# Performance work log

Hardware: AMD Instinct MI355X
Metric: run time of the kernel (lower is better)

Reference implementation:

```python
import jax, jax.numpy as jnp
import numpy as np


def lstm_cell(x, h, c, Wih, Whh, bih, bhh):
    # PyTorch LSTM gate order: i, f, g, o
    gates = x @ Wih.T + h @ Whh.T + bih + bhh
    i, f, g, o = jnp.split(gates, 4, axis=-1)
    c_new = jax.nn.sigmoid(f) * c + jax.nn.sigmoid(i) * jnp.tanh(g)
    h_new = jax.nn.sigmoid(o) * jnp.tanh(c_new)
    return h_new, c_new


def setup_inputs() -> dict:
    V, E, H, L, S, B, T = 100000, 256, 256, 2, 256, 16, 128
    G = 4 * H
    s = 0.1  # weight scale to keep activations/gradients well-conditioned
    key = jax.random.key(0)
    ks = jax.random.split(key, 16)
    return {
        'source': jax.random.randint(ks[0], (S, B), 0, V),
        'target_size': T,
        'target_embeddings': jax.random.normal(ks[1], (T, 1, E), dtype=jnp.float32),
        'h0': jax.random.normal(ks[2], (L, B, H), dtype=jnp.float32) * s,
        'c0': jax.random.normal(ks[3], (L, B, H), dtype=jnp.float32) * s,
        'embed_table': jax.random.normal(ks[4], (V, E), dtype=jnp.float32) * s,
        'enc_Wih': jax.random.normal(ks[5], (L, G, E), dtype=jnp.float32) * s,
        'enc_Whh': jax.random.normal(ks[6], (L, G, H), dtype=jnp.float32) * s,
        'enc_bih': jax.random.normal(ks[7], (L, G), dtype=jnp.float32) * s,
        'enc_bhh': jax.random.normal(ks[8], (L, G), dtype=jnp.float32) * s,
        'dec_Wih': jax.random.normal(ks[9], (L, G, E), dtype=jnp.float32) * s,
        'dec_Whh': jax.random.normal(ks[10], (L, G, H), dtype=jnp.float32) * s,
        'dec_bih': jax.random.normal(ks[11], (L, G), dtype=jnp.float32) * s,
        'dec_bhh': jax.random.normal(ks[12], (L, G), dtype=jnp.float32) * s,
        'attn_W': jax.random.normal(ks[13], (1, 2 * H), dtype=jnp.float32) * s,
        'attn_b': jnp.zeros((1,), dtype=jnp.float32),
        'comb_W': jax.random.normal(ks[14], (H, 2 * H), dtype=jnp.float32) * s,
        'comb_b': jnp.zeros((H,), dtype=jnp.float32),
    }


def reference(source, target_size, target_embeddings, h0, c0, embed_table,
              enc_Wih, enc_Whh, enc_bih, enc_bhh,
              dec_Wih, dec_Whh, dec_bih, dec_bhh,
              attn_W, attn_b, comb_W, comb_b):
    L = h0.shape[0]
    B = source.shape[1]

    # ---------------- encoder (per-step LSTM loop -> layer-wise scans) ----
    x = embed_table[source]  # [S, B, E]  (dropout is identity at eval)
    h_fin = []
    for l in range(L):
        def step(carry, xt, l=l):
            h, c = carry
            h, c = lstm_cell(xt, h, c, enc_Wih[l], enc_Whh[l], enc_bih[l], enc_bhh[l])
            return (h, c), h
        (hL, cL), x = jax.lax.scan(step, (h0[l], c0[l]), x)
        h_fin.append(hL)
    hidden_final = jnp.stack(h_fin)   # [L, B, H] == hiddens[-1] in the source
    enc_outputs = x                   # [S, B, H] last-layer hidden per step
    S = enc_outputs.shape[0]

    # NOTE (faithful to source bugs): seq2seq sets both decoder hidden AND
    # cell from encoder_hidden[-1], and the decoder runs its LSTM on the raw
    # input `embedding`, discarding the attention-combined output.
    x0 = jnp.tile(target_embeddings[0, 0], (B, 1))  # [B, E]

    def dec_step(carry, _):
        x, h, c = carry
        # per-step Bahdanau-style attention: computed but UNUSED, as in source
        cat = jnp.concatenate([jnp.broadcast_to(x, (S,) + x.shape), enc_outputs], axis=-1)
        w = jax.nn.softmax(cat @ attn_W.T + attn_b, axis=0)       # [S, B, 1]
        applied = (w * enc_outputs).sum(0)                         # [B, H]
        _combined = jax.nn.relu(jnp.concatenate([x, applied], axis=-1) @ comb_W.T + comb_b)
        # actual recurrence: multi-layer LSTM on the raw input x
        inp = x
        hs, cs = [], []
        for l in range(h.shape[0]):
            hl, cl = lstm_cell(inp, h[l], c[l], dec_Wih[l], dec_Whh[l], dec_bih[l], dec_bhh[l])
            hs.append(hl)
            cs.append(cl)
            inp = hl
        return (inp, jnp.stack(hs), jnp.stack(cs)), inp

    _, ys = jax.lax.scan(dec_step, (x0, hidden_final, hidden_final), None,
                         length=target_size - 1)  # ys: [T-1, B, H]
    H = ys.shape[-1]
    preds = jnp.zeros((target_size, 1, B, H), ys.dtype)
    preds = preds.at[1:].set(ys[:, None])  # predictions[0] stays zero
    return preds
```

## Files before the change

kernel.cpp:

```cpp
#include <hip/hip_runtime.h>
#include <hip/hip_bf16.h>

typedef __attribute__((ext_vector_type(8))) short short8;
typedef __attribute__((ext_vector_type(4))) float f32x4;

#define SEQ   256
#define BB    16
#define EE    256
#define HH    256
#define GG    1024
#define TT    128
#define NWG   32
#define KP    264
#define SLOT_S 8192
#define SENT  0xFF80FF80u
#define MAXTRY (1 << 20)

__device__ __forceinline__ float sigm(float x) { return 1.0f / (1.0f + __expf(-x)); }
__device__ __forceinline__ float tanh_f(float x) {
    float e = __expf(2.0f * x);
    return 1.0f - 2.0f / (e + 1.0f);
}
__device__ __forceinline__ void split2s(float v, short* hi, short* lo) {
    __hip_bfloat16 h = __float2bfloat16(v);
    __hip_bfloat16 l = __float2bfloat16(v - __bfloat162float(h));
    *hi = *(short*)&h; *lo = *(short*)&l;
}
__device__ __forceinline__ f32x4 MFMA(short8 a, short8 b, f32x4 c) {
    return __builtin_amdgcn_mfma_f32_16x16x32_bf16(a, b, c, 0, 0, 0);
}

__device__ __forceinline__ short8 ld16s(const short* p) {
    short8 r;
    asm volatile("global_load_dwordx4 %0, %1, off sc0 sc1" : "=v"(r) : "v"(p));
    return r;
}
__device__ __forceinline__ int ld4f(const int* p) {
    int r;
    asm volatile("global_load_dword %0, %1, off sc0 sc1\n\ts_waitcnt vmcnt(0)"
                 : "=v"(r) : "v"(p) : "memory");
    return r;
}
__device__ __forceinline__ void st4s(int* p, int v) {
    asm volatile("global_store_dword %0, %1, off sc0 sc1" :: "v"(p), "v"(v) : "memory");
}
__device__ __forceinline__ void vmwait() {
    asm volatile("s_waitcnt vmcnt(0)" ::: "memory");
    __builtin_amdgcn_sched_barrier(0);
}
__device__ __forceinline__ void sync_lds() {
    __builtin_amdgcn_sched_barrier(0);
    asm volatile("s_waitcnt lgkmcnt(0)" ::: "memory");
    __builtin_amdgcn_s_barrier();
    __builtin_amdgcn_sched_barrier(0);
}
union U8 { short8 s; unsigned u[4]; };
__device__ __forceinline__ unsigned chk(short8 f) {
    U8 x; x.s = f;
    return (unsigned)((x.u[0] == SENT) | (x.u[1] == SENT) | (x.u[2] == SENT) | (x.u[3] == SENT));
}

__global__ void k_sent(unsigned* p) {
    long i = ((long)blockIdx.x * 256 + threadIdx.x) * 4;
    p[i] = SENT; p[i + 1] = SENT; p[i + 2] = SENT; p[i + 3] = SENT;
}

__global__ void k_cvt4(const float* __restrict__ s0, const float* __restrict__ s1,
                       const float* __restrict__ s2, const float* __restrict__ s3,
                       char* __restrict__ ws) {
    int g = blockIdx.x >> 11;
    int i = (blockIdx.x & 2047) * 256 + threadIdx.x;
    const float* s = (g == 0) ? s0 : (g == 1) ? s1 : (g == 2) ? s2 : s3;
    __hip_bfloat16* hi = (__hip_bfloat16*)(ws + ((size_t)2 * g) * (1u << 20));
    __hip_bfloat16* lo = (__hip_bfloat16*)(ws + ((size_t)2 * g + 1) * (1u << 20));
    short a, b; split2s(s[i], &a, &b);
    hi[i] = *(__hip_bfloat16*)&a; lo[i] = *(__hip_bfloat16*)&b;
}

__global__ void k_embed(const int* __restrict__ src, const float* __restrict__ tab,
                        __hip_bfloat16* __restrict__ xhi, __hip_bfloat16* __restrict__ xlo) {
    int r = blockIdx.x;
    int j = threadIdx.x;
    long idx = src[r];
    short a, b; split2s(tab[idx * EE + j], &a, &b);
    xhi[(long)r * EE + j] = *(__hip_bfloat16*)&a;
    xlo[(long)r * EE + j] = *(__hip_bfloat16*)&b;
}

__global__ void __launch_bounds__(256) k_gemm_in(
        const __hip_bfloat16* __restrict__ Xhi, const __hip_bfloat16* __restrict__ Xlo,
        const __hip_bfloat16* __restrict__ Whi, const __hip_bfloat16* __restrict__ Wlo,
        const float* __restrict__ bih, const float* __restrict__ bhh,
        float* __restrict__ gates) {
    int lane = threadIdx.x & 63, w = threadIdx.x >> 6;
    int m0 = (blockIdx.x >> 4) * 16;
    int n0 = ((blockIdx.x & 15) * 4 + w) * 16;
    int cc = lane & 15, g = lane >> 4;
    int koff = g * 8;
    const short* xh = (const short*)Xhi + (long)(m0 + cc) * EE + koff;
    const short* xl = (const short*)Xlo + (long)(m0 + cc) * EE + koff;
    const short* wh = (const short*)Whi + (long)(n0 + cc) * EE + koff;
    const short* wl = (const short*)Wlo + (long)(n0 + cc) * EE + koff;
    f32x4 acc1 = {0.f, 0.f, 0.f, 0.f}, acc2 = {0.f, 0.f, 0.f, 0.f};
#pragma unroll
    for (int k = 0; k < EE; k += 32) {
        short8 ah = *(const short8*)(xh + k), al = *(const short8*)(xl + k);
        short8 bh = *(const short8*)(wh + k), bl = *(const short8*)(wl + k);
        acc1 = MFMA(ah, bh, acc1);
        acc2 = MFMA(ah, bl, acc2);
        acc2 = MFMA(al, bh, acc2);
    }
    f32x4 acc = acc1 + acc2;
    int ncol = n0 + cc;
    float bias = bih[ncol] + bhh[ncol];
    int jj = ncol & 255, qq = ncol >> 8;
    int mrow = m0 + g * 4;
#pragma unroll
    for (int r = 0; r < 4; ++r)
        gates[(long)(mrow + r) * GG + jj * 4 + qq] = acc[r] + bias;
}

__device__ __forceinline__ void load_wslice(const short* __restrict__ Wg, int j0,
                                            short* __restrict__ Wl) {
    int tid = threadIdx.x;
    int lr = tid >> 3;
    int q = lr >> 3, jl = lr & 7;
    const short* src = Wg + (long)(q * 256 + j0 + jl) * 256;
    short* dst = Wl + lr * KP;
#pragma unroll
    for (int s = 0; s < 4; ++s) {
        int c = (tid & 7) * 8 + s * 64;
        *(short8*)(dst + c) = *(const short8*)(src + c);
    }
}


__global__ void __launch_bounds__(256, 1) k_enc_coop(
        const float* __restrict__ gates0,
        const short* __restrict__ Whh0h, const short* __restrict__ Whh0l,
        const short* __restrict__ Wih1h, const short* __restrict__ Wih1l,
        const short* __restrict__ Whh1h, const short* __restrict__ Whh1l,
        const float* __restrict__ bih1, const float* __restrict__ bhh1,
        const float* __restrict__ h0p, const float* __restrict__ c0p,
        short* __restrict__ H0, short* __restrict__ H1,
        float* __restrict__ hfin,
        int* __restrict__ FE0, int* __restrict__ FE1) {
    __shared__ short Wl[6][32 * KP];
    __shared__ float gacc[2][8][16][17];

    int tid = threadIdx.x, bid = blockIdx.x;
    int j0 = bid * 8;
    load_wslice(Whh0h, j0, Wl[0]); load_wslice(Whh0l, j0, Wl[1]);
    load_wslice(Wih1h, j0, Wl[2]); load_wslice(Wih1l, j0, Wl[3]);
    load_wslice(Whh1h, j0, Wl[4]); load_wslice(Whh1l, j0, Wl[5]);

    int bb = (tid & 127) >> 3, jl = tid & 7, j = j0 + jl, lay = tid >> 7;
    float creg = c0p[lay * 4096 + bb * 256 + j];
    float bs[4] = {0.f, 0.f, 0.f, 0.f};
    if (lay) {
#pragma unroll
        for (int q = 0; q < 4; ++q) bs[q] = bih1[q * 256 + j] + bhh1[q * 256 + j];
    }
    f32x4 gnew = {0.f, 0.f, 0.f, 0.f};
    if (!lay) {
        gnew = *(const f32x4*)(gates0 + ((long)bb * 256 + j) * 4);
    }
    {
        float hv = h0p[lay * 4096 + bb * 256 + j];
        short sh, sl; split2s(hv, &sh, &sl);
        int mh = (unsigned short)sh, ml = (unsigned short)sl;
        int nh = __shfl_down(mh, 1), nl = __shfl_down(ml, 1);
        int* dst = (int*)(lay ? H1 : H0);
        if (!(jl & 1)) {
            int idx = bb * 256 + bid * 8 + (jl >> 1);
            st4s(dst + idx, mh | (nh << 16));
            st4s(dst + idx + 4, ml | (nl << 16));
        }
    }
    __syncthreads();
    if (tid == 0) { st4s(FE0 + bid, 1); st4s(FE1 + bid, 1); }

    int lane = tid & 63, w = tid >> 6, cc = lane & 15, g4 = lane >> 4;
    int tw = w & 1, kb = (w >> 1) * 128;
    int abase = cc * 512 + kb * 2 + g4 * 16;
    int wr = (tw * 16 + cc) * KP + kb + (g4 * 8);

    for (int i = 0; i <= SEQ; ++i) {
        bool actL0 = (i < SEQ), actL1 = (i >= 1);
        int par = i & 1;

        if (tid >= 192) {
            int ln = tid - 192;
            const int* fp = (ln < 32) ? (FE0 + (long)i * 32 + ln)
                                      : (FE1 + (long)(i - 1) * 32 + (ln - 32));
            bool active = (ln < 32) ? true : actL1;
            int tries = 0;
            while (true) {
                int v = active ? ld4f(fp) : 1;
                if (__all(v != (int)SENT) || ++tries > MAXTRY) break;
            }
        }
        sync_lds();

        short8 f0h[4], f0l[4], f1h[4], f1l[4];
        const short* b0 = H0 + (long)i * SLOT_S + abase;
        const short* b1 = H1 + (long)(i - 1) * SLOT_S + abase;
        int tries = 0;
        while (true) {
#pragma unroll
            for (int ki = 0; ki < 4; ++ki) {
                f0h[ki] = ld16s(b0 + ki * 64);
                f0l[ki] = ld16s(b0 + ki * 64 + 8);
            }
            if (actL1) {
#pragma unroll
                for (int ki = 0; ki < 4; ++ki) {
                    f1h[ki] = ld16s(b1 + ki * 64);
                    f1l[ki] = ld16s(b1 + ki * 64 + 8);
                }
            }
            vmwait();
            unsigned bad = 0;
#pragma unroll
            for (int ki = 0; ki < 4; ++ki) bad |= chk(f0h[ki]) | chk(f0l[ki]);
            if (actL1) {
#pragma unroll
                for (int ki = 0; ki < 4; ++ki) bad |= chk(f1h[ki]) | chk(f1l[ki]);
            }
            if (!__any((int)bad) || ++tries > MAXTRY) break;
        }

        float gpre[4] = {0.f, 0.f, 0.f, 0.f};
        if (!lay) {
#pragma unroll
            for (int q = 0; q < 4; ++q) gpre[q] = gnew[q];
        }

        f32x4 z = {0.f, 0.f, 0.f, 0.f};
        f32x4 s0 = z, s1 = z;
        if (actL0) {
            f32x4 a1 = z, a2 = z;
#pragma unroll
            for (int ki = 0; ki < 4; ++ki) {
                short8 wh  = *(const short8*)(Wl[0] + wr + ki * 32);
                short8 wl2 = *(const short8*)(Wl[1] + wr + ki * 32);
                a1 = MFMA(f0h[ki], wh, a1);
                a2 = MFMA(f0h[ki], wl2, a2);
                a2 = MFMA(f0l[ki], wh, a2);
            }
            s0 = a1 + a2;
        }
        if (actL1) {
            f32x4 a1 = z, a2 = z;
#pragma unroll
            for (int ki = 0; ki < 4; ++ki) {
                a1 = MFMA(f0h[ki], *(const short8*)(Wl[2] + wr + ki * 32), a1);
                a2 = MFMA(f0h[ki], *(const short8*)(Wl[3] + wr + ki * 32), a2);
                a2 = MFMA(f0l[ki], *(const short8*)(Wl[2] + wr + ki * 32), a2);
                a1 = MFMA(f1h[ki], *(const short8*)(Wl[4] + wr + ki * 32), a1);
                a2 = MFMA(f1h[ki], *(const short8*)(Wl[5] + wr + ki * 32), a2);
                a2 = MFMA(f1l[ki], *(const short8*)(Wl[4] + wr + ki * 32), a2);
            }
            s1 = a1 + a2;
        }
#pragma unroll
        for (int r = 0; r < 4; ++r) {
            gacc[par][w][g4 * 4 + r][cc] = s0[r];
            gacc[par][4 + w][g4 * 4 + r][cc] = s1[r];
        }
        sync_lds();

        bool act = lay ? actL1 : actL0;
        if (act) {
            int t = lay ? (i - 1) : i;
            float gv[4];
#pragma unroll
            for (int q = 0; q < 4; ++q) {
                int lr = q * 8 + jl, tl = lr >> 4, c = lr & 15;
                gv[q] = lay ? (gacc[par][4 + tl][bb][c] + gacc[par][6 + tl][bb][c] + bs[q])
                            : (gacc[par][tl][bb][c] + gacc[par][2 + tl][bb][c] + gpre[q]);
            }
            float c = sigm(gv[1]) * creg + sigm(gv[0]) * tanh_f(gv[2]);
            creg = c;
            float h = sigm(gv[3]) * tanh_f(c);
            short sh, sl; split2s(h, &sh, &sl);
            int mh = (unsigned short)sh, ml = (unsigned short)sl;
            int nh = __shfl_down(mh, 1), nl = __shfl_down(ml, 1);
            int* dst = (int*)(lay ? (H1 + (long)i * SLOT_S) : (H0 + (long)(i + 1) * SLOT_S));
            if (!(jl & 1)) {
                int idx = bb * 256 + bid * 8 + (jl >> 1);
                st4s(dst + idx, mh | (nh << 16));
                st4s(dst + idx + 4, ml | (nl << 16));
            }
            if (t == SEQ - 1) hfin[lay * 4096 + bb * 256 + j] = h;
        }

        __syncthreads();
        if (tid == 0) {
            if (actL0) st4s(FE0 + (long)(i + 1) * 32 + bid, 1);
            if (actL1) st4s(FE1 + (long)i * 32 + bid, 1);
        }
        if (!lay && i + 1 < SEQ)
            gnew = *(const f32x4*)(gates0 + ((long)((i + 1) * BB + bb) * 256 + j) * 4);
    }
}

__global__ void __launch_bounds__(256, 1) k_dec_coop(
        const short* __restrict__ Wihh, const short* __restrict__ Wihl,
        const short* __restrict__ Whhh, const short* __restrict__ Whhl,
        const float* __restrict__ dbih, const float* __restrict__ dbhh,
        const float* __restrict__ tef, const float* __restrict__ hfin,
        short* __restrict__ H0, short* __restrict__ H1,
        short* __restrict__ TE,
        float* __restrict__ preds,
        int* __restrict__ FD0, int* __restrict__ FD1, int* __restrict__ FT) {
    __shared__ short Wl[8][32 * KP];
    __shared__ float gacc[2][4][16][17];
    const int WN = GG * EE;

    int tid = threadIdx.x, bid = blockIdx.x;
    int j0 = bid * 8;
    load_wslice(Wihh, j0, Wl[0]);      load_wslice(Wihl, j0, Wl[1]);
    load_wslice(Whhh, j0, Wl[2]);      load_wslice(Whhl, j0, Wl[3]);
    load_wslice(Wihh + WN, j0, Wl[4]); load_wslice(Wihl + WN, j0, Wl[5]);
    load_wslice(Whhh + WN, j0, Wl[6]); load_wslice(Whhl + WN, j0, Wl[7]);

    int bb = (tid & 127) >> 3, jl = tid & 7, j = j0 + jl;
    float c0r = 0.f, c1r = 0.f;
    float bs0[4] = {0,0,0,0}, bs1[4] = {0,0,0,0};
    if (tid < 128) {
        float h0v = hfin[bb * 256 + j], h1v = hfin[4096 + bb * 256 + j];
        c0r = h0v; c1r = h1v;
        preds[bb * 256 + j] = 0.0f;
        int idx = bb * 256 + bid * 8 + (jl >> 1);
        short sh, sl;
        split2s(tef[j], &sh, &sl);
        {
            int mh = (unsigned short)sh, ml = (unsigned short)sl;
            int nh = __shfl_down(mh, 1), nl = __shfl_down(ml, 1);
            if (!(jl & 1)) { st4s((int*)TE + idx, mh | (nh << 16));
                             st4s((int*)TE + idx + 4, ml | (nl << 16)); }
        }
        split2s(h0v, &sh, &sl);
        {
            int mh = (unsigned short)sh, ml = (unsigned short)sl;
            int nh = __shfl_down(mh, 1), nl = __shfl_down(ml, 1);
            if (!(jl & 1)) { st4s((int*)H0 + idx, mh | (nh << 16));
                             st4s((int*)H0 + idx + 4, ml | (nl << 16)); }
        }
        split2s(h1v, &sh, &sl);
        {
            int mh = (unsigned short)sh, ml = (unsigned short)sl;
            int nh = __shfl_down(mh, 1), nl = __shfl_down(ml, 1);
            if (!(jl & 1)) { st4s((int*)H1 + idx, mh | (nh << 16));
                             st4s((int*)H1 + idx + 4, ml | (nl << 16)); }
        }
#pragma unroll
        for (int q = 0; q < 4; ++q) {
            bs0[q] = dbih[q*256+j] + dbhh[q*256+j];
            bs1[q] = dbih[GG + q*256+j] + dbhh[GG + q*256+j];
        }
    }
    __syncthreads();
    if (tid == 0) { st4s(FT + bid, 1); st4s(FD0 + bid, 1); st4s(FD1 + bid, 1); }

    int lane = tid & 63, w = tid >> 6, cc = lane & 15, g4 = lane >> 4;
    int tw = w & 1, kb = (w >> 1) * 128;
    int abase = cc * 512 + kb * 2 + g4 * 16;
    int wr = (tw * 16 + cc) * KP + kb + (g4 * 8);

    short8 xAh[4], xAl[4], xBh[4], xBl[4], h1ih[4], h1il[4];

    {
        if (tid >= 192) {
            int ln = tid - 192;
            const int* fp = (ln < 32) ? (FD0 + ln) : (FD1 + (ln - 32));
            int tries = 0;
            while (true) {
                int v = ld4f(fp);
                if (__all(v != (int)SENT) || ++tries > MAXTRY) break;
            }
        }
        sync_lds();
        const short* p0 = H0 + abase;
        const short* p1 = H1 + abase;
        int tries = 0;
        while (true) {
#pragma unroll
            for (int ki = 0; ki < 4; ++ki) {
                xBh[ki] = ld16s(p0 + ki * 64); xBl[ki] = ld16s(p0 + ki * 64 + 8);
                h1ih[ki] = ld16s(p1 + ki * 64); h1il[ki] = ld16s(p1 + ki * 64 + 8);
            }
            vmwait();
            unsigned bad = 0;
#pragma unroll
            for (int ki = 0; ki < 4; ++ki)
                bad |= chk(xBh[ki]) | chk(xBl[ki]) | chk(h1ih[ki]) | chk(h1il[ki]);
            if (!__any((int)bad) || ++tries > MAXTRY) break;
        }
    }

    for (int t = 0; t < TT - 1; ++t) {
        {
            if (tid >= 192) {
                int ln = tid - 192;
                const int* fp = t ? (FD1 + (long)t * 32 + ln) : (FT + ln);
                int tries = 0;
                while (true) {
                    int v = (ln < 32) ? ld4f(fp) : 1;
                    if (__all(v != (int)SENT) || ++tries > MAXTRY) break;
                }
            }
            sync_lds();
            const short* px = (t ? H1 + (long)t * SLOT_S : TE) + abase;
            int tries = 0;
            while (true) {
#pragma unroll
                for (int ki = 0; ki < 4; ++ki) {
                    xAh[ki] = ld16s(px + ki * 64); xAl[ki] = ld16s(px + ki * 64 + 8);
                }
                vmwait();
                unsigned bad = 0;
#pragma unroll
                for (int ki = 0; ki < 4; ++ki) bad |= chk(xAh[ki]) | chk(xAl[ki]);
                if (!__any((int)bad) || ++tries > MAXTRY) break;
            }
            f32x4 a1 = {0.f,0.f,0.f,0.f}, a2 = {0.f,0.f,0.f,0.f};
#pragma unroll
            for (int ki = 0; ki < 4; ++ki) {
                a1 = MFMA(xAh[ki], *(const short8*)(Wl[0] + wr + ki * 32), a1);
                a2 = MFMA(xAh[ki], *(const short8*)(Wl[1] + wr + ki * 32), a2);
                a2 = MFMA(xAl[ki], *(const short8*)(Wl[0] + wr + ki * 32), a2);
                a1 = MFMA(xBh[ki], *(const short8*)(Wl[2] + wr + ki * 32), a1);
                a2 = MFMA(xBh[ki], *(const short8*)(Wl[3] + wr + ki * 32), a2);
                a2 = MFMA(xBl[ki], *(const short8*)(Wl[2] + wr + ki * 32), a2);
            }
            f32x4 accs = a1 + a2;
#pragma unroll
            for (int r = 0; r < 4; ++r) gacc[0][w][g4 * 4 + r][cc] = accs[r];
        }
        sync_lds();
        if (tid < 128) {
            float gv[4];
#pragma unroll
            for (int q = 0; q < 4; ++q) {
                int lr = q * 8 + jl;
                gv[q] = gacc[0][lr >> 4][bb][lr & 15] + gacc[0][2 + (lr >> 4)][bb][lr & 15] + bs0[q];
            }
            float c = sigm(gv[1]) * c0r + sigm(gv[0]) * tanh_f(gv[2]);
            c0r = c;
            float h = sigm(gv[3]) * tanh_f(c);
            short sh, sl; split2s(h, &sh, &sl);
            int mh = (unsigned short)sh, ml = (unsigned short)sl;
            int nh = __shfl_down(mh, 1), nl = __shfl_down(ml, 1);
            if (!(jl & 1)) {
                int idx = bb * 256 + bid * 8 + (jl >> 1);
                int* dst = (int*)(H0 + (long)(t + 1) * SLOT_S);
                st4s(dst + idx, mh | (nh << 16));
                st4s(dst + idx + 4, ml | (nl << 16));
            }
        }
        __syncthreads();
        if (tid == 0) st4s(FD0 + (long)(t + 1) * 32 + bid, 1);

        {
            if (tid >= 192) {
                int ln = tid - 192;
                const int* fp = FD0 + (long)(t + 1) * 32 + ln;
                int tries = 0;
                while (true) {
                    int v = (ln < 32) ? ld4f(fp) : 1;
                    if (__all(v != (int)SENT) || ++tries > MAXTRY) break;
                }
            }
            sync_lds();
            const short* px = H0 + (long)(t + 1) * SLOT_S + abase;
            int tries = 0;
            while (true) {
#pragma unroll
                for (int ki = 0; ki < 4; ++ki) {
                    xBh[ki] = ld16s(px + ki * 64); xBl[ki] = ld16s(px + ki * 64 + 8);
                }
                vmwait();
                unsigned bad = 0;
#pragma unroll
                for (int ki = 0; ki < 4; ++ki) bad |= chk(xBh[ki]) | chk(xBl[ki]);
                if (!__any((int)bad) || ++tries > MAXTRY) break;
            }
            f32x4 a1 = {0.f,0.f,0.f,0.f}, a2 = {0.f,0.f,0.f,0.f};
#pragma unroll
            for (int ki = 0; ki < 4; ++ki) {
                short8 hh = t ? xAh[ki] : h1ih[ki];
                short8 hl = t ? xAl[ki] : h1il[ki];
                a1 = MFMA(xBh[ki], *(const short8*)(Wl[4] + wr + ki * 32), a1);
                a2 = MFMA(xBh[ki], *(const short8*)(Wl[5] + wr + ki * 32), a2);
                a2 = MFMA(xBl[ki], *(const short8*)(Wl[4] + wr + ki * 32), a2);
                a1 = MFMA(hh, *(const short8*)(Wl[6] + wr + ki * 32), a1);
                a2 = MFMA(hh, *(const short8*)(Wl[7] + wr + ki * 32), a2);
                a2 = MFMA(hl, *(const short8*)(Wl[6] + wr + ki * 32), a2);
            }
            f32x4 accs = a1 + a2;
#pragma unroll
            for (int r = 0; r < 4; ++r) gacc[1][w][g4 * 4 + r][cc] = accs[r];
        }
        sync_lds();
        if (tid < 128) {
            float gv[4];
#pragma unroll
            for (int q = 0; q < 4; ++q) {
                int lr = q * 8 + jl;
                gv[q] = gacc[1][lr >> 4][bb][lr & 15] + gacc[1][2 + (lr >> 4)][bb][lr & 15] + bs1[q];
            }
            float c = sigm(gv[1]) * c1r + sigm(gv[0]) * tanh_f(gv[2]);
            c1r = c;
            float h = sigm(gv[3]) * tanh_f(c);
            short sh, sl; split2s(h, &sh, &sl);
            int mh = (unsigned short)sh, ml = (unsigned short)sl;
            int nh = __shfl_down(mh, 1), nl = __shfl_down(ml, 1);
            if (!(jl & 1)) {
                int idx = bb * 256 + bid * 8 + (jl >> 1);
                int* dst = (int*)(H1 + (long)(t + 1) * SLOT_S);
                st4s(dst + idx, mh | (nh << 16));
                st4s(dst + idx + 4, ml | (nl << 16));
            }
            preds[((long)(t + 1) * BB + bb) * HH + j] = h;
        }
        __syncthreads();
        if (tid == 0) st4s(FD1 + (long)(t + 1) * 32 + bid, 1);
    }
}

extern "C" void kernel_launch(void* const* d_in, const int* in_sizes, int n_in,
                              void* d_out, int out_size, void* d_ws, size_t ws_size,
                              hipStream_t stream) {
    const int*   src   = (const int*)  d_in[0];
    const float* te    = (const float*)d_in[2];
    const float* h0    = (const float*)d_in[3];
    const float* c0    = (const float*)d_in[4];
    const float* table = (const float*)d_in[5];
    const float* eWih  = (const float*)d_in[6];
    const float* eWhh  = (const float*)d_in[7];
    const float* ebih  = (const float*)d_in[8];
    const float* ebhh  = (const float*)d_in[9];
    const float* dWih  = (const float*)d_in[10];
    const float* dWhh  = (const float*)d_in[11];
    const float* dbih  = (const float*)d_in[12];
    const float* dbhh  = (const float*)d_in[13];
    float* preds = (float*)d_out;

    const int WN = GG * EE;
    const size_t MB = 1u << 20;
    char* ws = (char*)d_ws;
    short* eWih_hi = (short*)(ws + 0 * MB);
    short* eWih_lo = (short*)(ws + 1 * MB);
    short* eWhh_hi = (short*)(ws + 2 * MB);
    short* eWhh_lo = (short*)(ws + 3 * MB);
    short* dWih_hi = (short*)(ws + 4 * MB);
    short* dWih_lo = (short*)(ws + 5 * MB);
    short* dWhh_hi = (short*)(ws + 6 * MB);
    short* dWhh_lo = (short*)(ws + 7 * MB);
    short* Xa_hi   = (short*)(ws + 8 * MB);
    short* Xa_lo   = (short*)(ws + 10 * MB);
    float* hfin    = (float*)(ws + 12 * MB);
    short* slots   = (short*)(ws + 13 * MB);
    short* SLe0 = slots;
    short* SLe1 = SLe0 + (long)257 * SLOT_S;
    short* SLd0 = SLe1 + (long)257 * SLOT_S;
    short* SLd1 = SLd0 + (long)128 * SLOT_S;
    short* SLte = SLd1 + (long)128 * SLOT_S;
    int*   FL   = (int*)(SLte + (long)1 * SLOT_S);
    int* FE0 = FL;
    int* FE1 = FL + 257 * 32;
    int* FD0 = FE1 + 257 * 32;
    int* FD1 = FD0 + 128 * 32;
    int* FT  = FD1 + 128 * 32;
    float* gates0 = (float*)(ws + 26 * MB);

    k_sent<<<3109, 256, 0, stream>>>((unsigned*)slots);

    k_cvt4<<<8192, 256, 0, stream>>>(eWih, eWhh, dWih, dWhh, ws);

    k_embed<<<4096, 256, 0, stream>>>(src, table, (__hip_bfloat16*)Xa_hi, (__hip_bfloat16*)Xa_lo);
    k_gemm_in<<<4096, 256, 0, stream>>>((__hip_bfloat16*)Xa_hi, (__hip_bfloat16*)Xa_lo,
                                        (__hip_bfloat16*)eWih_hi, (__hip_bfloat16*)eWih_lo,
                                        ebih, ebhh, gates0);
    k_enc_coop<<<NWG, 256, 0, stream>>>(gates0, eWhh_hi, eWhh_lo,
                                        eWih_hi + WN, eWih_lo + WN, eWhh_hi + WN, eWhh_lo + WN,
                                        ebih + GG, ebhh + GG, h0, c0,
                                        SLe0, SLe1, hfin, FE0, FE1);

    k_dec_coop<<<NWG, 256, 0, stream>>>(dWih_hi, dWih_lo, dWhh_hi, dWhh_lo,
                                        dbih, dbhh, te, hfin,
                                        SLd0, SLd1, SLte, preds, FD0, FD1, FT);
    (void)in_sizes; (void)n_in; (void)out_size; (void)ws_size;
}
```

Before: 2.122 ms.

## Split encoder layers across separate workgroups with per-wave completion flags

The persistent encoder kernel previously ran both LSTM layers in one workgroup per column slice, skewed by one step and joined by a block-wide barrier. It now launches twice as many workgroups: half run layer 0 and half run layer 1, each with its own weight slices and its own step loop. Completion flags are widened to two per workgroup and set per wave after a vmcnt wait, which removes the trailing __syncthreads before signalling. The intent is to shorten the per-step critical path and let layer 0 run ahead of layer 1. In exchange, layer 1 must spin on layer-0 flags, and the kernel needs 64 co-resident workgroups.

```diff
diff --git a/kernel.cpp b/kernel.cpp
--- a/kernel.cpp
+++ b/kernel.cpp
@@ -146,100 +146,87 @@
         float* __restrict__ hfin,
         int* __restrict__ FE0, int* __restrict__ FE1) {
     __shared__ short Wl[6][32 * KP];
-    __shared__ float gacc[2][8][16][17];
+    __shared__ float gacc[2][4][16][17];
 
     int tid = threadIdx.x, bid = blockIdx.x;
-    int j0 = bid * 8;
-    load_wslice(Whh0h, j0, Wl[0]); load_wslice(Whh0l, j0, Wl[1]);
-    load_wslice(Wih1h, j0, Wl[2]); load_wslice(Wih1l, j0, Wl[3]);
-    load_wslice(Whh1h, j0, Wl[4]); load_wslice(Whh1l, j0, Wl[5]);
-
-    int bb = (tid & 127) >> 3, jl = tid & 7, j = j0 + jl, lay = tid >> 7;
-    float creg = c0p[lay * 4096 + bb * 256 + j];
+    bool isL0 = (bid < NWG);
+    int gb = bid & 31;
+    int j0 = gb * 8;
+    if (isL0) {
+        load_wslice(Whh0h, j0, Wl[0]); load_wslice(Whh0l, j0, Wl[1]);
+    } else {
+        load_wslice(Wih1h, j0, Wl[2]); load_wslice(Wih1l, j0, Wl[3]);
+        load_wslice(Whh1h, j0, Wl[4]); load_wslice(Whh1l, j0, Wl[5]);
+    }
+
+    int bb = (tid & 127) >> 3, jl = tid & 7, j = j0 + jl;
+    float creg = 0.f;
     float bs[4] = {0.f, 0.f, 0.f, 0.f};
-    if (lay) {
-#pragma unroll
-        for (int q = 0; q < 4; ++q) bs[q] = bih1[q * 256 + j] + bhh1[q * 256 + j];
-    }
     f32x4 gnew = {0.f, 0.f, 0.f, 0.f};
-    if (!lay) {
-        gnew = *(const f32x4*)(gates0 + ((long)bb * 256 + j) * 4);
-    }
-    {
-        float hv = h0p[lay * 4096 + bb * 256 + j];
+    if (tid < 128) {
+        int off = (isL0 ? 0 : 4096) + bb * 256 + j;
+        creg = c0p[off];
+        if (!isL0) {
+#pragma unroll
+            for (int q = 0; q < 4; ++q) bs[q] = bih1[q * 256 + j] + bhh1[q * 256 + j];
+        } else {
+            gnew = *(const f32x4*)(gates0 + ((long)bb * 256 + j) * 4);
+        }
+        float hv = h0p[off];
         short sh, sl; split2s(hv, &sh, &sl);
         int mh = (unsigned short)sh, ml = (unsigned short)sl;
         int nh = __shfl_down(mh, 1), nl = __shfl_down(ml, 1);
-        int* dst = (int*)(lay ? H1 : H0);
+        int* dst = (int*)(isL0 ? H0 : H1);
         if (!(jl & 1)) {
-            int idx = bb * 256 + bid * 8 + (jl >> 1);
+            int idx = bb * 256 + gb * 8 + (jl >> 1);
             st4s(dst + idx, mh | (nh << 16));
             st4s(dst + idx + 4, ml | (nl << 16));
         }
     }
     __syncthreads();
-    if (tid == 0) { st4s(FE0 + bid, 1); st4s(FE1 + bid, 1); }
+    if (tid == 0) {
+        int* F = isL0 ? FE0 : FE1;
+        st4s(F + gb * 2, 1); st4s(F + gb * 2 + 1, 1);
+    }
 
     int lane = tid & 63, w = tid >> 6, cc = lane & 15, g4 = lane >> 4;
     int tw = w & 1, kb = (w >> 1) * 128;
     int abase = cc * 512 + kb * 2 + g4 * 16;
     int wr = (tw * 16 + cc) * KP + kb + (g4 * 8);
 
-    for (int i = 0; i <= SEQ; ++i) {
-        bool actL0 = (i < SEQ), actL1 = (i >= 1);
-        int par = i & 1;
-
-        if (tid >= 192) {
-            int ln = tid - 192;
-            const int* fp = (ln < 32) ? (FE0 + (long)i * 32 + ln)
-                                      : (FE1 + (long)(i - 1) * 32 + (ln - 32));
-            bool active = (ln < 32) ? true : actL1;
+    if (isL0) {
+        for (int t = 0; t < SEQ; ++t) {
+            int par = t & 1;
+            if (tid >= 192) {
+                int ln = tid - 192;
+                const int* fp = FE0 + (long)t * 64 + ln;
+                int tries = 0;
+                while (true) {
+                    int v = ld4f(fp);
+                    if (__all(v != (int)SENT) || ++tries > MAXTRY) break;
+                }
+            }
+            sync_lds();
+            short8 f0h[4], f0l[4];
+            const short* b0 = H0 + (long)t * SLOT_S + abase;
             int tries = 0;
             while (true) {
-                int v = active ? ld4f(fp) : 1;
-                if (__all(v != (int)SENT) || ++tries > MAXTRY) break;
-            }
-        }
-        sync_lds();
-
-        short8 f0h[4], f0l[4], f1h[4], f1l[4];
-        const short* b0 = H0 + (long)i * SLOT_S + abase;
-        const short* b1 = H1 + (long)(i - 1) * SLOT_S + abase;
-        int tries = 0;
-        while (true) {
-#pragma unroll
-            for (int ki = 0; ki < 4; ++ki) {
-                f0h[ki] = ld16s(b0 + ki * 64);
-                f0l[ki] = ld16s(b0 + ki * 64 + 8);
-            }
-            if (actL1) {
 #pragma unroll
                 for (int ki = 0; ki < 4; ++ki) {
-                    f1h[ki] = ld16s(b1 + ki * 64);
-                    f1l[ki] = ld16s(b1 + ki * 64 + 8);
-                }
-            }
-            vmwait();
-            unsigned bad = 0;
-#pragma unroll
-            for (int ki = 0; ki < 4; ++ki) bad |= chk(f0h[ki]) | chk(f0l[ki]);
-            if (actL1) {
-#pragma unroll
-                for (int ki = 0; ki < 4; ++ki) bad |= chk(f1h[ki]) | chk(f1l[ki]);
-            }
-            if (!__any((int)bad) || ++tries > MAXTRY) break;
-        }
-
-        float gpre[4] = {0.f, 0.f, 0.f, 0.f};
-        if (!lay) {
+                    f0h[ki] = ld16s(b0 + ki * 64);
+                    f0l[ki] = ld16s(b0 + ki * 64 + 8);
+                }
+                vmwait();
+                unsigned bad = 0;
+#pragma unroll
+                for (int ki = 0; ki < 4; ++ki) bad |= chk(f0h[ki]) | chk(f0l[ki]);
+                if (!__any((int)bad) || ++tries > MAXTRY) break;
+            }
+            float gpre[4];
 #pragma unroll
             for (int q = 0; q < 4; ++q) gpre[q] = gnew[q];
-        }
-
-        f32x4 z = {0.f, 0.f, 0.f, 0.f};
-        f32x4 s0 = z, s1 = z;
-        if (actL0) {
-            f32x4 a1 = z, a2 = z;
+
+            f32x4 a1 = {0.f,0.f,0.f,0.f}, a2 = {0.f,0.f,0.f,0.f};
 #pragma unroll
             for (int ki = 0; ki < 4; ++ki) {
                 short8 wh  = *(const short8*)(Wl[0] + wr + ki * 32);
@@ -248,10 +235,73 @@
                 a2 = MFMA(f0h[ki], wl2, a2);
                 a2 = MFMA(f0l[ki], wh, a2);
             }
-            s0 = a1 + a2;
-        }
-        if (actL1) {
-            f32x4 a1 = z, a2 = z;
+            f32x4 s0 = a1 + a2;
+#pragma unroll
+            for (int r = 0; r < 4; ++r) gacc[par][w][g4 * 4 + r][cc] = s0[r];
+            sync_lds();
+            if (tid < 128) {
+                float gv[4];
+#pragma unroll
+                for (int q = 0; q < 4; ++q) {
+                    int lr = q * 8 + jl, tl = lr >> 4, c = lr & 15;
+                    gv[q] = gacc[par][tl][bb][c] + gacc[par][2 + tl][bb][c] + gpre[q];
+                }
+                float c = sigm(gv[1]) * creg + sigm(gv[0]) * tanh_f(gv[2]);
+                creg = c;
+                float h = sigm(gv[3]) * tanh_f(c);
+                short sh, sl; split2s(h, &sh, &sl);
+                int mh = (unsigned short)sh, ml = (unsigned short)sl;
+                int nh = __shfl_down(mh, 1), nl = __shfl_down(ml, 1);
+                int* dst = (int*)(H0 + (long)(t + 1) * SLOT_S);
+                if (!(jl & 1)) {
+                    int idx = bb * 256 + gb * 8 + (jl >> 1);
+                    st4s(dst + idx, mh | (nh << 16));
+                    st4s(dst + idx + 4, ml | (nl << 16));
+                }
+                asm volatile("s_waitcnt vmcnt(0)" ::: "memory");
+                __builtin_amdgcn_sched_barrier(0);
+                if ((tid & 63) == 0)
+                    st4s(FE0 + (long)(t + 1) * 64 + gb * 2 + (tid >> 6), 1);
+                if (t == SEQ - 1) hfin[bb * 256 + j] = h;
+                if (t + 1 < SEQ)
+                    gnew = *(const f32x4*)(gates0 + ((long)((t + 1) * BB + bb) * 256 + j) * 4);
+            }
+        }
+    } else {
+        for (int t = 0; t < SEQ; ++t) {
+            int par = t & 1;
+            if (tid >= 192) {
+                int ln = tid - 192;
+                const int* fp0 = FE0 + (long)(t + 1) * 64 + ln;
+                const int* fp1 = FE1 + (long)t * 64 + ln;
+                int tries = 0;
+                while (true) {
+                    int v0 = ld4f(fp0);
+                    int v1 = ld4f(fp1);
+                    if (__all((v0 != (int)SENT) && (v1 != (int)SENT)) || ++tries > MAXTRY) break;
+                }
+            }
+            sync_lds();
+            short8 f0h[4], f0l[4], f1h[4], f1l[4];
+            const short* b0 = H0 + (long)(t + 1) * SLOT_S + abase;
+            const short* b1 = H1 + (long)t * SLOT_S + abase;
+            int tries = 0;
+            while (true) {
+#pragma unroll
+                for (int ki = 0; ki < 4; ++ki) {
+                    f0h[ki] = ld16s(b0 + ki * 64);
+                    f0l[ki] = ld16s(b0 + ki * 64 + 8);
+                    f1h[ki] = ld16s(b1 + ki * 64);
+                    f1l[ki] = ld16s(b1 + ki * 64 + 8);
+                }
+                vmwait();
+                unsigned bad = 0;
+#pragma unroll
+                for (int ki = 0; ki < 4; ++ki)
+                    bad |= chk(f0h[ki]) | chk(f0l[ki]) | chk(f1h[ki]) | chk(f1l[ki]);
+                if (!__any((int)bad) || ++tries > MAXTRY) break;
+            }
+            f32x4 a1 = {0.f,0.f,0.f,0.f}, a2 = {0.f,0.f,0.f,0.f};
 #pragma unroll
             for (int ki = 0; ki < 4; ++ki) {
                 a1 = MFMA(f0h[ki], *(const short8*)(Wl[2] + wr + ki * 32), a1);
@@ -261,47 +311,36 @@
                 a2 = MFMA(f1h[ki], *(const short8*)(Wl[5] + wr + ki * 32), a2);
                 a2 = MFMA(f1l[ki], *(const short8*)(Wl[4] + wr + ki * 32), a2);
             }
-            s1 = a1 + a2;
-        }
-#pragma unroll
-        for (int r = 0; r < 4; ++r) {
-            gacc[par][w][g4 * 4 + r][cc] = s0[r];
-            gacc[par][4 + w][g4 * 4 + r][cc] = s1[r];
-        }
-        sync_lds();
-
-        bool act = lay ? actL1 : actL0;
-        if (act) {
-            int t = lay ? (i - 1) : i;
-            float gv[4];
-#pragma unroll
-            for (int q = 0; q < 4; ++q) {
-                int lr = q * 8 + jl, tl = lr >> 4, c = lr & 15;
-                gv[q] = lay ? (gacc[par][4 + tl][bb][c] + gacc[par][6 + tl][bb][c] + bs[q])
-                            : (gacc[par][tl][bb][c] + gacc[par][2 + tl][bb][c] + gpre[q]);
-            }
-            float c = sigm(gv[1]) * creg + sigm(gv[0]) * tanh_f(gv[2]);
-            creg = c;
-            float h = sigm(gv[3]) * tanh_f(c);
-            short sh, sl; split2s(h, &sh, &sl);
-            int mh = (unsigned short)sh, ml = (unsigned short)sl;
-            int nh = __shfl_down(mh, 1), nl = __shfl_down(ml, 1);
-            int* dst = (int*)(lay ? (H1 + (long)i * SLOT_S) : (H0 + (long)(i + 1) * SLOT_S));
-            if (!(jl & 1)) {
-                int idx = bb * 256 + bid * 8 + (jl >> 1);
-                st4s(dst + idx, mh | (nh << 16));
-                st4s(dst + idx + 4, ml | (nl << 16));
-            }
-            if (t == SEQ - 1) hfin[lay * 4096 + bb * 256 + j] = h;
-        }
-
-        __syncthreads();
-        if (tid == 0) {
-            if (actL0) st4s(FE0 + (long)(i + 1) * 32 + bid, 1);
-            if (actL1) st4s(FE1 + (long)i * 32 + bid, 1);
-        }
-        if (!lay && i + 1 < SEQ)
-            gnew = *(const f32x4*)(gates0 + ((long)((i + 1) * BB + bb) * 256 + j) * 4);
+            f32x4 s1 = a1 + a2;
+#pragma unroll
+            for (int r = 0; r < 4; ++r) gacc[par][w][g4 * 4 + r][cc] = s1[r];
+            sync_lds();
+            if (tid < 128) {
+                float gv[4];
+#pragma unroll
+                for (int q = 0; q < 4; ++q) {
+                    int lr = q * 8 + jl, tl = lr >> 4, c = lr & 15;
+                    gv[q] = gacc[par][tl][bb][c] + gacc[par][2 + tl][bb][c] + bs[q];
+                }
+                float c = sigm(gv[1]) * creg + sigm(gv[0]) * tanh_f(gv[2]);
+                creg = c;
+                float h = sigm(gv[3]) * tanh_f(c);
+                short sh, sl; split2s(h, &sh, &sl);
+                int mh = (unsigned short)sh, ml = (unsigned short)sl;
+                int nh = __shfl_down(mh, 1), nl = __shfl_down(ml, 1);
+                int* dst = (int*)(H1 + (long)(t + 1) * SLOT_S);
+                if (!(jl & 1)) {
+                    int idx = bb * 256 + gb * 8 + (jl >> 1);
+                    st4s(dst + idx, mh | (nh << 16));
+                    st4s(dst + idx + 4, ml | (nl << 16));
+                }
+                asm volatile("s_waitcnt vmcnt(0)" ::: "memory");
+                __builtin_amdgcn_sched_barrier(0);
+                if ((tid & 63) == 0)
+                    st4s(FE1 + (long)(t + 1) * 64 + gb * 2 + (tid >> 6), 1);
+                if (t == SEQ - 1) hfin[4096 + bb * 256 + j] = h;
+            }
+        }
     }
 }
 
@@ -570,13 +609,13 @@
     short* SLte = SLd1 + (long)128 * SLOT_S;
     int*   FL   = (int*)(SLte + (long)1 * SLOT_S);
     int* FE0 = FL;
-    int* FE1 = FL + 257 * 32;
-    int* FD0 = FE1 + 257 * 32;
+    int* FE1 = FE0 + 257 * 64;
+    int* FD0 = FE1 + 257 * 64;
     int* FD1 = FD0 + 128 * 32;
     int* FT  = FD1 + 128 * 32;
     float* gates0 = (float*)(ws + 26 * MB);
 
-    k_sent<<<3109, 256, 0, stream>>>((unsigned*)slots);
+    k_sent<<<3125, 256, 0, stream>>>((unsigned*)slots);
 
     k_cvt4<<<8192, 256, 0, stream>>>(eWih, eWhh, dWih, dWhh, ws);
 
@@ -584,7 +623,7 @@
     k_gemm_in<<<4096, 256, 0, stream>>>((__hip_bfloat16*)Xa_hi, (__hip_bfloat16*)Xa_lo,
                                         (__hip_bfloat16*)eWih_hi, (__hip_bfloat16*)eWih_lo,
                                         ebih, ebhh, gates0);
-    k_enc_coop<<<NWG, 256, 0, stream>>>(gates0, eWhh_hi, eWhh_lo,
+    k_enc_coop<<<2 * NWG, 256, 0, stream>>>(gates0, eWhh_hi, eWhh_lo,
                                         eWih_hi + WN, eWih_lo + WN, eWhh_hi + WN, eWhh_lo + WN,
                                         ebih + GG, ebhh + GG, h0, c0,
                                         SLe0, SLe1, hfin, FE0, FE1);
```

Result: slower. 2.449 ms (+15.5%).

## Replace per-block barrier+flag with per-wave completion flags in LSTM recurrences

Applied to the files above, without the earlier changes.

Each wave that writes h now waits for its own stores and publishes its own ready flag, instead of the whole block hitting __syncthreads before thread 0 sets a single per-block flag. Flag arrays double to 64 entries per step, and pollers check both layer flags with paired loads. The goal is to drop a block-wide barrier from the critical path of each recurrent step so consumers can start sooner. The cost is twice as many flag stores and polls, plus a larger sentinel init region.

```diff
diff --git a/kernel.cpp b/kernel.cpp
--- a/kernel.cpp
+++ b/kernel.cpp
@@ -40,6 +40,14 @@
     asm volatile("global_load_dword %0, %1, off sc0 sc1\n\ts_waitcnt vmcnt(0)"
                  : "=v"(r) : "v"(p) : "memory");
     return r;
+}
+__device__ __forceinline__ void ld4f2(const int* p0, const int* p1, int* v0, int* v1) {
+    int a, b;
+    asm volatile("global_load_dword %0, %2, off sc0 sc1\n\t"
+                 "global_load_dword %1, %3, off sc0 sc1\n\t"
+                 "s_waitcnt vmcnt(0)"
+                 : "=&v"(a), "=&v"(b) : "v"(p0), "v"(p1) : "memory");
+    *v0 = a; *v1 = b;
 }
 __device__ __forceinline__ void st4s(int* p, int v) {
     asm volatile("global_store_dword %0, %1, off sc0 sc1" :: "v"(p), "v"(v) : "memory");
@@ -178,7 +186,10 @@
         }
     }
     __syncthreads();
-    if (tid == 0) { st4s(FE0 + bid, 1); st4s(FE1 + bid, 1); }
+    if (tid == 0) {
+        st4s(FE0 + bid * 2, 1); st4s(FE0 + bid * 2 + 1, 1);
+        st4s(FE1 + bid * 2, 1); st4s(FE1 + bid * 2 + 1, 1);
+    }
 
     int lane = tid & 63, w = tid >> 6, cc = lane & 15, g4 = lane >> 4;
     int tw = w & 1, kb = (w >> 1) * 128;
@@ -191,13 +202,14 @@
 
         if (tid >= 192) {
             int ln = tid - 192;
-            const int* fp = (ln < 32) ? (FE0 + (long)i * 32 + ln)
-                                      : (FE1 + (long)(i - 1) * 32 + (ln - 32));
-            bool active = (ln < 32) ? true : actL1;
+            const int* fp0 = FE0 + (long)i * 64 + ln;
+            const int* fp1 = actL1 ? (FE1 + (long)(i - 1) * 64 + ln) : fp0;
             int tries = 0;
             while (true) {
-                int v = active ? ld4f(fp) : 1;
-                if (__all(v != (int)SENT) || ++tries > MAXTRY) break;
+                int v0, v1;
+                ld4f2(fp0, fp1, &v0, &v1);
+                if (!actL1) v1 = 1;
+                if (__all((v0 != (int)SENT) && (v1 != (int)SENT)) || ++tries > MAXTRY) break;
             }
         }
         sync_lds();
@@ -292,16 +304,17 @@
                 st4s(dst + idx, mh | (nh << 16));
                 st4s(dst + idx + 4, ml | (nl << 16));
             }
+            asm volatile("s_waitcnt vmcnt(0)" ::: "memory");
+            __builtin_amdgcn_sched_barrier(0);
+            if ((tid & 63) == 0) {
+                int wv = tid >> 6;
+                if (!lay) st4s(FE0 + (long)(i + 1) * 64 + bid * 2 + wv, 1);
+                else      st4s(FE1 + (long)i * 64 + bid * 2 + (wv - 2), 1);
+            }
             if (t == SEQ - 1) hfin[lay * 4096 + bb * 256 + j] = h;
-        }
-
-        __syncthreads();
-        if (tid == 0) {
-            if (actL0) st4s(FE0 + (long)(i + 1) * 32 + bid, 1);
-            if (actL1) st4s(FE1 + (long)i * 32 + bid, 1);
-        }
-        if (!lay && i + 1 < SEQ)
-            gnew = *(const f32x4*)(gates0 + ((long)((i + 1) * BB + bb) * 256 + j) * 4);
+            if (!lay && i + 1 < SEQ)
+                gnew = *(const f32x4*)(gates0 + ((long)((i + 1) * BB + bb) * 256 + j) * 4);
+        }
     }
 }
 
@@ -362,7 +375,11 @@
         }
     }
     __syncthreads();
-    if (tid == 0) { st4s(FT + bid, 1); st4s(FD0 + bid, 1); st4s(FD1 + bid, 1); }
+    if (tid == 0) {
+        st4s(FT + bid * 2, 1);  st4s(FT + bid * 2 + 1, 1);
+        st4s(FD0 + bid * 2, 1); st4s(FD0 + bid * 2 + 1, 1);
+        st4s(FD1 + bid * 2, 1); st4s(FD1 + bid * 2 + 1, 1);
+    }
 
     int lane = tid & 63, w = tid >> 6, cc = lane & 15, g4 = lane >> 4;
     int tw = w & 1, kb = (w >> 1) * 128;
@@ -374,11 +391,13 @@
     {
         if (tid >= 192) {
             int ln = tid - 192;
-            const int* fp = (ln < 32) ? (FD0 + ln) : (FD1 + (ln - 32));
+            const int* fp0 = FD0 + ln;
+            const int* fp1 = FD1 + ln;
             int tries = 0;
             while (true) {
-                int v = ld4f(fp);
-                if (__all(v != (int)SENT) || ++tries > MAXTRY) break;
+                int v0, v1;
+                ld4f2(fp0, fp1, &v0, &v1);
+                if (__all((v0 != (int)SENT) && (v1 != (int)SENT)) || ++tries > MAXTRY) break;
             }
         }
         sync_lds();
@@ -404,10 +423,10 @@
         {
             if (tid >= 192) {
                 int ln = tid - 192;
-                const int* fp = t ? (FD1 + (long)t * 32 + ln) : (FT + ln);
+                const int* fp = t ? (FD1 + (long)t * 64 + ln) : (FT + ln);
                 int tries = 0;
                 while (true) {
-                    int v = (ln < 32) ? ld4f(fp) : 1;
+                    int v = ld4f(fp);
                     if (__all(v != (int)SENT) || ++tries > MAXTRY) break;
                 }
             }
@@ -459,17 +478,19 @@
                 st4s(dst + idx, mh | (nh << 16));
                 st4s(dst + idx + 4, ml | (nl << 16));
             }
-        }
-        __syncthreads();
-        if (tid == 0) st4s(FD0 + (long)(t + 1) * 32 + bid, 1);
+            asm volatile("s_waitcnt vmcnt(0)" ::: "memory");
+            __builtin_amdgcn_sched_barrier(0);
+            if ((tid & 63) == 0)
+                st4s(FD0 + (long)(t + 1) * 64 + bid * 2 + (tid >> 6), 1);
+        }
 
         {
             if (tid >= 192) {
                 int ln = tid - 192;
-                const int* fp = FD0 + (long)(t + 1) * 32 + ln;
+                const int* fp = FD0 + (long)(t + 1) * 64 + ln;
                 int tries = 0;
                 while (true) {
-                    int v = (ln < 32) ? ld4f(fp) : 1;
+                    int v = ld4f(fp);
                     if (__all(v != (int)SENT) || ++tries > MAXTRY) break;
                 }
             }
@@ -523,10 +544,12 @@
                 st4s(dst + idx, mh | (nh << 16));
                 st4s(dst + idx + 4, ml | (nl << 16));
             }
+            asm volatile("s_waitcnt vmcnt(0)" ::: "memory");
+            __builtin_amdgcn_sched_barrier(0);
+            if ((tid & 63) == 0)
+                st4s(FD1 + (long)(t + 1) * 64 + bid * 2 + (tid >> 6), 1);
             preds[((long)(t + 1) * BB + bb) * HH + j] = h;
         }
-        __syncthreads();
-        if (tid == 0) st4s(FD1 + (long)(t + 1) * 32 + bid, 1);
     }
 }
 
@@ -570,13 +593,13 @@
     short* SLte = SLd1 + (long)128 * SLOT_S;
     int*   FL   = (int*)(SLte + (long)1 * SLOT_S);
     int* FE0 = FL;
-    int* FE1 = FL + 257 * 32;
-    int* FD0 = FE1 + 257 * 32;
-    int* FD1 = FD0 + 128 * 32;
-    int* FT  = FD1 + 128 * 32;
+    int* FE1 = FE0 + 257 * 64;
+    int* FD0 = FE1 + 257 * 64;
+    int* FD1 = FD0 + 128 * 64;
+    int* FT  = FD1 + 128 * 64;
     float* gates0 = (float*)(ws + 26 * MB);
 
-    k_sent<<<3109, 256, 0, stream>>>((unsigned*)slots);
+    k_sent<<<3133, 256, 0, stream>>>((unsigned*)slots);
 
     k_cvt4<<<8192, 256, 0, stream>>>(eWih, eWhh, dWih, dWhh, ws);
 
```

New measurement: 2.728 ms. 28.6% more time.
